# Kernel tuning notes

Hardware: AMD Instinct MI355X
Metric: run time of the kernel (lower is better)

The kernel has to match this reference:

```python
import jax, jax.numpy as jnp
import numpy as np

VOCAB, E, H = 100000, 300, 2048

def setup_inputs() -> dict:
    key = jax.random.key(0)
    k1, k2, k3, k4, k5, k6 = jax.random.split(key, 6)
    s_e = 1.0 / np.sqrt(H)
    return {
        "input": jax.random.randint(k1, (128, 64), 0, VOCAB),
        "embed": jax.random.normal(k2, (VOCAB, E), dtype=jnp.float32),
        "w_ih": jax.random.normal(k3, (4 * H, E), dtype=jnp.float32) * s_e,
        "w_hh": jax.random.normal(k4, (4 * H, H), dtype=jnp.float32) * s_e,
        "b_ih": jax.random.normal(k5, (4 * H,), dtype=jnp.float32) * s_e,
        "b_hh": jax.random.normal(k6, (4 * H,), dtype=jnp.float32) * s_e,
    }

def _lstm_cell(x, h, c, w_ih, w_hh, b_ih, b_hh):
    # PyTorch LSTMCell: gates = x @ W_ih^T + b_ih + h @ W_hh^T + b_hh
    gates = x @ w_ih.T + b_ih + h @ w_hh.T + b_hh  # [B, 4H]
    i, f, g, o = jnp.split(gates, 4, axis=-1)
    i, f, o = jax.nn.sigmoid(i), jax.nn.sigmoid(f), jax.nn.sigmoid(o)
    g = jnp.tanh(g)
    c_new = f * c + i * g
    h_new = o * jnp.tanh(c_new)
    return h_new, c_new

def reference(input, embed, w_ih, w_hh, b_ih, b_hh):
    B, T = input.shape
    x = embed[input]  # [B, T, E] embedding lookup
    x_t = jnp.swapaxes(x, 0, 1)  # [T, B, E] for scan over time
    h0 = jnp.zeros((B, H), dtype=x.dtype)
    c0 = jnp.zeros((B, H), dtype=x.dtype)

    def step(carry, xt):
        h, c = carry
        h, c = _lstm_cell(xt, h, c, w_ih, w_hh, b_ih, b_hh)
        return (h, c), None

    (hT, cT), _ = jax.lax.scan(step, (h0, c0), x_t)
    return hT  # [B, H]
```

## Files before the change

### kernel.cpp

```cpp
#include <hip/hip_runtime.h>
#include <stdint.h>

#define H_    2048
#define B_    128
#define T_    64
#define E_    300
#define NKU   76
#define XGRP  48
#define NWG   256
#define NTHR  512

typedef unsigned short u16;
typedef uint32_t u32;
typedef short bf8 __attribute__((ext_vector_type(8)));
typedef float f4 __attribute__((ext_vector_type(4)));

__device__ __forceinline__ u16 f2b(float f) {
    u32 u = __float_as_uint(f);
    u += 0x7fffu + ((u >> 16) & 1u);
    return (u16)(u >> 16);
}
__device__ __forceinline__ float sigm(float x) { return 1.f / (1.f + __expf(-x)); }
__device__ __forceinline__ float tanh_(float x) {
    float xx = fminf(fmaxf(x, -15.f), 15.f);
    float e = __expf(2.f * xx);
    return (e - 1.f) / (e + 1.f);
}

__global__ void prep_kernel(const float* __restrict__ w_hh, const float* __restrict__ w_ih,
                            const float* __restrict__ b_ih, const float* __restrict__ b_hh,
                            u16* __restrict__ wP, float* __restrict__ bsP,
                            float* __restrict__ cP, u16* __restrict__ hP0) {
    int tid = blockIdx.x * blockDim.x + threadIdx.x;
    int np = gridDim.x * blockDim.x;
    const int NF = NWG * NKU * 2 * 64;
    for (int f = tid; f < NF; f += np) {
        int lane = f & 63;
        int fr = f >> 6;
        int nt = fr & 1;
        int rest = fr >> 1;
        int ku = rest % NKU;
        int wg = rest / NKU;
        int l15 = lane & 15, q = lane >> 4;
        int nl = nt * 16 + l15;
        int g = nl & 3, jj = nl >> 2;
        int ng = g * H_ + wg * 8 + jj;
        int k0 = ku * 32 + q * 8;
        union { u16 s[8]; uint4 v; } tmp;
#pragma unroll
        for (int j = 0; j < 8; ++j) {
            int k = k0 + j;
            float v;
            if (k < H_) v = w_hh[(size_t)ng * H_ + k];
            else { int kx = k - H_; v = (kx < E_) ? w_ih[(size_t)ng * E_ + kx] : 0.f; }
            tmp.s[j] = f2b(v);
        }
        *(uint4*)&wP[(size_t)f * 8] = tmp.v;
    }
    for (int n = tid; n < 4 * H_; n += np) {
        int wg = n >> 5, nl = n & 31;
        int jj = nl >> 2, g = nl & 3;
        int src = g * H_ + wg * 8 + jj;
        bsP[n] = b_ih[src] + b_hh[src];
    }
    for (int i = tid; i < NWG * B_ * 8; i += np) cP[i] = 0.f;
    for (int i = tid; i < (H_ / 8) * B_ * 8 / 2; i += np) ((u32*)hP0)[i] = 0u;
}

__global__ void gather_kernel(const int* __restrict__ input, const float* __restrict__ embed,
                              u16* __restrict__ xP) {
    int t = blockIdx.x;
    u16* xt = xP + (size_t)t * XGRP * B_ * 8;
    for (int id = threadIdx.x; id < XGRP * B_; id += blockDim.x) {
        int b = id & (B_ - 1);
        int gx = id >> 7;
        int row = input[b * T_ + t];
        const float* src = embed + (size_t)row * E_;
        union { u16 s[8]; uint4 v; } tmp;
#pragma unroll
        for (int j = 0; j < 8; ++j) {
            int k = gx * 8 + j;
            tmp.s[j] = (k < E_) ? f2b(src[k]) : (u16)0;
        }
        *(uint4*)&xt[(size_t)id * 8] = tmp.v;
    }
}

__global__ __launch_bounds__(NTHR) void
step_kernel(const u16* __restrict__ wP, const float* __restrict__ bsP,
            const u16* __restrict__ xt, const u16* __restrict__ hin,
            u16* __restrict__ hout, float* __restrict__ cP,
            float* __restrict__ outp) {
    __shared__ float bufs[8][32][36];
    int tid = threadIdx.x;
    int wid = tid >> 6, lane = tid & 63;
    int l15 = lane & 15, q = lane >> 4;
    int wg = blockIdx.x;

    int cnt = (wid < 4) ? 10 : 9;
    int ks  = (wid < 4) ? wid * 10 : 40 + (wid - 4) * 9;

    const u16* wbase = wP + (size_t)wg * NKU * 1024 + lane * 8;
    int hoff = q * 1024 + l15 * 8;

    f4 acc[2][8];
#pragma unroll
    for (int nt = 0; nt < 2; ++nt)
#pragma unroll
        for (int mt = 0; mt < 8; ++mt) acc[nt][mt] = (f4)0.f;

#define LDF(KU, WF, HB) do {                                                  \
        int ku_ = (KU);                                                       \
        const u16* wb_ = wbase + (size_t)ku_ * 1024;                          \
        WF[0] = *(const bf8*)wb_;                                             \
        WF[1] = *(const bf8*)(wb_ + 512);                                     \
        const u16* hb_ = ((ku_ < 64) ? (hin + (size_t)ku_ * 4096)             \
                                     : (xt + (size_t)(ku_ - 64) * 4096)) + hoff; \
        _Pragma("unroll")                                                     \
        for (int mt_ = 0; mt_ < 8; ++mt_) HB[mt_] = *(const bf8*)(hb_ + mt_ * 128); \
    } while (0)

#define MM(WF, HB) do {                                                       \
        _Pragma("unroll")                                                     \
        for (int mt_ = 0; mt_ < 8; ++mt_) {                                   \
            acc[0][mt_] = __builtin_amdgcn_mfma_f32_16x16x32_bf16(WF[0], HB[mt_], acc[0][mt_], 0, 0, 0); \
            acc[1][mt_] = __builtin_amdgcn_mfma_f32_16x16x32_bf16(WF[1], HB[mt_], acc[1][mt_], 0, 0, 0); \
        }                                                                     \
    } while (0)

    bf8 wfA[2], hbA[8], wfB[2], hbB[8];
    LDF(ks, wfA, hbA);
    int i = 0;
    while (true) {
        if (i + 1 < cnt) LDF(ks + i + 1, wfB, hbB);
        MM(wfA, hbA);
        if (i + 1 >= cnt) break;
        if (i + 2 < cnt) LDF(ks + i + 2, wfA, hbA);
        MM(wfB, hbB);
        if (i + 2 >= cnt) break;
        i += 2;
    }
#undef LDF
#undef MM

    int cjj = tid & 7, cml = (tid >> 3) & 31;
    f4 bsv = {0.f, 0.f, 0.f, 0.f};
    if (tid < 256) bsv = *(const f4*)&bsP[wg * 32 + cjj * 4];
#pragma unroll
    for (int p = 0; p < 4; ++p) {
        __syncthreads();
#pragma unroll
        for (int mh = 0; mh < 2; ++mh) {
            int mt = p * 2 + mh;
            int ml = mh * 16 + l15;
            *(f4*)&bufs[wid][ml][q * 4]      = acc[0][mt];
            *(f4*)&bufs[wid][ml][16 + q * 4] = acc[1][mt];
        }
        __syncthreads();
        if (tid < 256) {
            int m = p * 32 + cml;
            f4 s = {0.f, 0.f, 0.f, 0.f};
#pragma unroll
            for (int kp = 0; kp < 8; ++kp) {
                f4 v = *(const f4*)&bufs[kp][cml][cjj * 4];
                s[0] += v[0]; s[1] += v[1]; s[2] += v[2]; s[3] += v[3];
            }
            float iv = sigm(s[0] + bsv[0]);
            float fv = sigm(s[1] + bsv[1]);
            float gv = tanh_(s[2] + bsv[2]);
            float ov = sigm(s[3] + bsv[3]);
            size_t ci = ((size_t)wg * B_ + m) * 8 + cjj;
            float cn = fv * cP[ci] + iv * gv;
            cP[ci] = cn;
            float hn = ov * tanh_(cn);
            hout[ci] = f2b(hn);
            if (outp) outp[(size_t)m * H_ + wg * 8 + cjj] = hn;
        }
    }
}

extern "C" void kernel_launch(void* const* d_in, const int* in_sizes, int n_in,
                              void* d_out, int out_size, void* d_ws, size_t ws_size,
                              hipStream_t stream) {
    const int*   input = (const int*)d_in[0];
    const float* embed = (const float*)d_in[1];
    const float* w_ih  = (const float*)d_in[2];
    const float* w_hh  = (const float*)d_in[3];
    const float* b_ih  = (const float*)d_in[4];
    const float* b_hh  = (const float*)d_in[5];
    float* out = (float*)d_out;

    char* ws = (char*)d_ws;
    size_t o = 0;
    u16* wP   = (u16*)(ws + o); o += (size_t)NWG * NKU * 2 * 64 * 8 * 2;
    u16* xP   = (u16*)(ws + o); o += (size_t)T_ * XGRP * B_ * 8 * 2;
    u16* hP0  = (u16*)(ws + o); o += (size_t)(H_ / 8) * B_ * 8 * 2;
    u16* hP1  = (u16*)(ws + o); o += (size_t)(H_ / 8) * B_ * 8 * 2;
    float* cP = (float*)(ws + o); o += (size_t)NWG * B_ * 8 * 4;
    float* bsP = (float*)(ws + o); o += (size_t)4 * H_ * 4;

    prep_kernel<<<2048, 256, 0, stream>>>(w_hh, w_ih, b_ih, b_hh, wP, bsP, cP, hP0);
    gather_kernel<<<T_, 256, 0, stream>>>(input, embed, xP);

    for (int t = 0; t < T_; ++t) {
        const u16* hin = (t & 1) ? hP1 : hP0;
        u16* hout      = (t & 1) ? hP0 : hP1;
        float* hof     = (t == T_ - 1) ? out : nullptr;
        step_kernel<<<NWG, NTHR, 0, stream>>>(
            wP, bsP, xP + (size_t)t * XGRP * B_ * 8, hin, hout, cP, hof);
    }
}
```

Baseline: 1.127 ms.

## Retile LSTM step to 64 gate columns by 64 batch rows per workgroup

```diff
diff --git a/kernel.cpp b/kernel.cpp
--- a/kernel.cpp
+++ b/kernel.cpp
@@ -9,6 +9,7 @@
 #define XGRP  48
 #define NWG   256
 #define NTHR  512
+#define NJG   128
 
 typedef unsigned short u16;
 typedef uint32_t u32;
@@ -33,18 +34,18 @@
                             float* __restrict__ cP, u16* __restrict__ hP0) {
     int tid = blockIdx.x * blockDim.x + threadIdx.x;
     int np = gridDim.x * blockDim.x;
-    const int NF = NWG * NKU * 2 * 64;
+    const int NF = NJG * NKU * 4 * 64;
     for (int f = tid; f < NF; f += np) {
         int lane = f & 63;
         int fr = f >> 6;
-        int nt = fr & 1;
-        int rest = fr >> 1;
+        int nt = fr & 3;
+        int rest = fr >> 2;
         int ku = rest % NKU;
-        int wg = rest / NKU;
+        int jg = rest / NKU;
         int l15 = lane & 15, q = lane >> 4;
         int nl = nt * 16 + l15;
         int g = nl & 3, jj = nl >> 2;
-        int ng = g * H_ + wg * 8 + jj;
+        int ng = g * H_ + jg * 16 + jj;
         int k0 = ku * 32 + q * 8;
         union { u16 s[8]; uint4 v; } tmp;
 #pragma unroll
@@ -57,13 +58,13 @@
         }
         *(uint4*)&wP[(size_t)f * 8] = tmp.v;
     }
-    for (int n = tid; n < 4 * H_; n += np) {
-        int wg = n >> 5, nl = n & 31;
-        int jj = nl >> 2, g = nl & 3;
-        int src = g * H_ + wg * 8 + jj;
+    for (int n = tid; n < NJG * 64; n += np) {
+        int jg = n >> 6, r = n & 63;
+        int jj = r >> 2, g = r & 3;
+        int src = g * H_ + jg * 16 + jj;
         bsP[n] = b_ih[src] + b_hh[src];
     }
-    for (int i = tid; i < NWG * B_ * 8; i += np) cP[i] = 0.f;
+    for (int i = tid; i < NJG * B_ * 16; i += np) cP[i] = 0.f;
     for (int i = tid; i < (H_ / 8) * B_ * 8 / 2; i += np) ((u32*)hP0)[i] = 0u;
 }
 
@@ -91,90 +92,98 @@
             const u16* __restrict__ xt, const u16* __restrict__ hin,
             u16* __restrict__ hout, float* __restrict__ cP,
             float* __restrict__ outp) {
-    __shared__ float bufs[8][32][36];
+    __shared__ float bufs[8][16][68];
     int tid = threadIdx.x;
     int wid = tid >> 6, lane = tid & 63;
     int l15 = lane & 15, q = lane >> 4;
-    int wg = blockIdx.x;
+    int jg  = blockIdx.x & 127;
+    int wgm = blockIdx.x >> 7;
 
     int cnt = (wid < 4) ? 10 : 9;
     int ks  = (wid < 4) ? wid * 10 : 40 + (wid - 4) * 9;
 
-    const u16* wbase = wP + (size_t)wg * NKU * 1024 + lane * 8;
-    int hoff = q * 1024 + l15 * 8;
-
-    f4 acc[2][8];
-#pragma unroll
-    for (int nt = 0; nt < 2; ++nt)
-#pragma unroll
-        for (int mt = 0; mt < 8; ++mt) acc[nt][mt] = (f4)0.f;
+    const u16* wbase = wP + (size_t)jg * NKU * 2048 + lane * 8;
+    int hoff = q * 1024 + wgm * 512 + l15 * 8;
+
+    f4 acc[4][4];
+#pragma unroll
+    for (int nt = 0; nt < 4; ++nt)
+#pragma unroll
+        for (int mt = 0; mt < 4; ++mt) acc[nt][mt] = (f4)0.f;
 
 #define LDF(KU, WF, HB) do {                                                  \
         int ku_ = (KU);                                                       \
-        const u16* wb_ = wbase + (size_t)ku_ * 1024;                          \
-        WF[0] = *(const bf8*)wb_;                                             \
+        const u16* wb_ = wbase + (size_t)ku_ * 2048;                          \
+        WF[0] = *(const bf8*)(wb_);                                           \
         WF[1] = *(const bf8*)(wb_ + 512);                                     \
+        WF[2] = *(const bf8*)(wb_ + 1024);                                    \
+        WF[3] = *(const bf8*)(wb_ + 1536);                                    \
         const u16* hb_ = ((ku_ < 64) ? (hin + (size_t)ku_ * 4096)             \
                                      : (xt + (size_t)(ku_ - 64) * 4096)) + hoff; \
-        _Pragma("unroll")                                                     \
-        for (int mt_ = 0; mt_ < 8; ++mt_) HB[mt_] = *(const bf8*)(hb_ + mt_ * 128); \
+        HB[0] = *(const bf8*)(hb_);                                           \
+        HB[1] = *(const bf8*)(hb_ + 128);                                     \
+        HB[2] = *(const bf8*)(hb_ + 256);                                     \
+        HB[3] = *(const bf8*)(hb_ + 384);                                     \
     } while (0)
 
 #define MM(WF, HB) do {                                                       \
         _Pragma("unroll")                                                     \
-        for (int mt_ = 0; mt_ < 8; ++mt_) {                                   \
-            acc[0][mt_] = __builtin_amdgcn_mfma_f32_16x16x32_bf16(WF[0], HB[mt_], acc[0][mt_], 0, 0, 0); \
-            acc[1][mt_] = __builtin_amdgcn_mfma_f32_16x16x32_bf16(WF[1], HB[mt_], acc[1][mt_], 0, 0, 0); \
-        }                                                                     \
+        for (int nt_ = 0; nt_ < 4; ++nt_)                                     \
+            _Pragma("unroll")                                                 \
+            for (int mt_ = 0; mt_ < 4; ++mt_)                                 \
+                acc[nt_][mt_] = __builtin_amdgcn_mfma_f32_16x16x32_bf16(      \
+                    WF[nt_], HB[mt_], acc[nt_][mt_], 0, 0, 0);                \
     } while (0)
 
-    bf8 wfA[2], hbA[8], wfB[2], hbB[8];
-    LDF(ks, wfA, hbA);
+    bf8 wA[4], hA[4], wB[4], hB[4], wC[4], hC[4];
+    LDF(ks, wA, hA);
+    LDF(ks + 1, wB, hB);
     int i = 0;
     while (true) {
-        if (i + 1 < cnt) LDF(ks + i + 1, wfB, hbB);
-        MM(wfA, hbA);
+        if (i + 2 < cnt) LDF(ks + i + 2, wC, hC);
+        MM(wA, hA);
         if (i + 1 >= cnt) break;
-        if (i + 2 < cnt) LDF(ks + i + 2, wfA, hbA);
-        MM(wfB, hbB);
+        if (i + 3 < cnt) LDF(ks + i + 3, wA, hA);
+        MM(wB, hB);
         if (i + 2 >= cnt) break;
-        i += 2;
+        if (i + 4 < cnt) LDF(ks + i + 4, wB, hB);
+        MM(wC, hC);
+        if (i + 3 >= cnt) break;
+        i += 3;
     }
 #undef LDF
 #undef MM
 
-    int cjj = tid & 7, cml = (tid >> 3) & 31;
+    int jj = tid & 15, ml16 = (tid >> 4) & 15;
     f4 bsv = {0.f, 0.f, 0.f, 0.f};
-    if (tid < 256) bsv = *(const f4*)&bsP[wg * 32 + cjj * 4];
+    if (tid < 256) bsv = *(const f4*)&bsP[jg * 64 + jj * 4];
 #pragma unroll
     for (int p = 0; p < 4; ++p) {
         __syncthreads();
-#pragma unroll
-        for (int mh = 0; mh < 2; ++mh) {
-            int mt = p * 2 + mh;
-            int ml = mh * 16 + l15;
-            *(f4*)&bufs[wid][ml][q * 4]      = acc[0][mt];
-            *(f4*)&bufs[wid][ml][16 + q * 4] = acc[1][mt];
-        }
+        *(f4*)&bufs[wid][l15][0 * 16 + q * 4] = acc[0][p];
+        *(f4*)&bufs[wid][l15][1 * 16 + q * 4] = acc[1][p];
+        *(f4*)&bufs[wid][l15][2 * 16 + q * 4] = acc[2][p];
+        *(f4*)&bufs[wid][l15][3 * 16 + q * 4] = acc[3][p];
         __syncthreads();
         if (tid < 256) {
-            int m = p * 32 + cml;
             f4 s = {0.f, 0.f, 0.f, 0.f};
 #pragma unroll
-            for (int kp = 0; kp < 8; ++kp) {
-                f4 v = *(const f4*)&bufs[kp][cml][cjj * 4];
+            for (int w = 0; w < 8; ++w) {
+                f4 v = *(const f4*)&bufs[w][ml16][jj * 4];
                 s[0] += v[0]; s[1] += v[1]; s[2] += v[2]; s[3] += v[3];
             }
             float iv = sigm(s[0] + bsv[0]);
             float fv = sigm(s[1] + bsv[1]);
             float gv = tanh_(s[2] + bsv[2]);
             float ov = sigm(s[3] + bsv[3]);
-            size_t ci = ((size_t)wg * B_ + m) * 8 + cjj;
+            int m = wgm * 64 + p * 16 + ml16;
+            size_t ci = ((size_t)jg * B_ + m) * 16 + jj;
             float cn = fv * cP[ci] + iv * gv;
             cP[ci] = cn;
             float hn = ov * tanh_(cn);
-            hout[ci] = f2b(hn);
-            if (outp) outp[(size_t)m * H_ + wg * 8 + cjj] = hn;
+            int jglob = jg * 16 + jj;
+            hout[(size_t)(jglob >> 3) * 1024 + m * 8 + (jglob & 7)] = f2b(hn);
+            if (outp) outp[(size_t)m * H_ + jglob] = hn;
         }
     }
 }
@@ -192,11 +201,11 @@
 
     char* ws = (char*)d_ws;
     size_t o = 0;
-    u16* wP   = (u16*)(ws + o); o += (size_t)NWG * NKU * 2 * 64 * 8 * 2;
+    u16* wP   = (u16*)(ws + o); o += (size_t)NJG * NKU * 4 * 64 * 8 * 2;
     u16* xP   = (u16*)(ws + o); o += (size_t)T_ * XGRP * B_ * 8 * 2;
     u16* hP0  = (u16*)(ws + o); o += (size_t)(H_ / 8) * B_ * 8 * 2;
     u16* hP1  = (u16*)(ws + o); o += (size_t)(H_ / 8) * B_ * 8 * 2;
-    float* cP = (float*)(ws + o); o += (size_t)NWG * B_ * 8 * 4;
+    float* cP = (float*)(ws + o); o += (size_t)NJG * B_ * 16 * 4;
     float* bsP = (float*)(ws + o); o += (size_t)4 * H_ * 4;
 
     prep_kernel<<<2048, 256, 0, stream>>>(w_hh, w_ih, b_ih, b_hh, wP, bsP, cP, hP0);
```

Result: faster. 1.074 ms (-4.7%).

## Fuse all timesteps into one persistent cooperative kernel with register-resident weights

Applied to the files above, without the earlier changes.

```diff
diff --git a/kernel.cpp b/kernel.cpp
--- a/kernel.cpp
+++ b/kernel.cpp
@@ -30,7 +30,7 @@
 __global__ void prep_kernel(const float* __restrict__ w_hh, const float* __restrict__ w_ih,
                             const float* __restrict__ b_ih, const float* __restrict__ b_hh,
                             u16* __restrict__ wP, float* __restrict__ bsP,
-                            float* __restrict__ cP, u16* __restrict__ hP0) {
+                            u16* __restrict__ hP0, unsigned* __restrict__ bar) {
     int tid = blockIdx.x * blockDim.x + threadIdx.x;
     int np = gridDim.x * blockDim.x;
     const int NF = NWG * NKU * 2 * 64;
@@ -57,14 +57,14 @@
         }
         *(uint4*)&wP[(size_t)f * 8] = tmp.v;
     }
-    for (int n = tid; n < 4 * H_; n += np) {
+    for (int n = tid; n < NWG * 32; n += np) {
         int wg = n >> 5, nl = n & 31;
         int jj = nl >> 2, g = nl & 3;
         int src = g * H_ + wg * 8 + jj;
         bsP[n] = b_ih[src] + b_hh[src];
     }
-    for (int i = tid; i < NWG * B_ * 8; i += np) cP[i] = 0.f;
     for (int i = tid; i < (H_ / 8) * B_ * 8 / 2; i += np) ((u32*)hP0)[i] = 0u;
+    for (int i = tid; i < 144; i += np) bar[i] = 0u;
 }
 
 __global__ void gather_kernel(const int* __restrict__ input, const float* __restrict__ embed,
@@ -86,12 +86,13 @@
     }
 }
 
-__global__ __launch_bounds__(NTHR) void
-step_kernel(const u16* __restrict__ wP, const float* __restrict__ bsP,
-            const u16* __restrict__ xt, const u16* __restrict__ hin,
-            u16* __restrict__ hout, float* __restrict__ cP,
-            float* __restrict__ outp) {
+__global__ __launch_bounds__(NTHR, 2) void
+lstm_persist(const u16* __restrict__ xb, const u16* __restrict__ wP,
+             const float* __restrict__ bsP, u16* __restrict__ h0,
+             u16* __restrict__ h1, unsigned* __restrict__ bar,
+             float* __restrict__ outp) {
     __shared__ float bufs[8][32][36];
+    __shared__ float cst[B_][8];
     int tid = threadIdx.x;
     int wid = tid >> 6, lane = tid & 63;
     int l15 = lane & 15, q = lane >> 4;
@@ -100,81 +101,123 @@
     int cnt = (wid < 4) ? 10 : 9;
     int ks  = (wid < 4) ? wid * 10 : 40 + (wid - 4) * 9;
 
-    const u16* wbase = wP + (size_t)wg * NKU * 1024 + lane * 8;
+    bf8 Wf[10][2];
+#pragma unroll
+    for (int i = 0; i < 10; ++i)
+        if (i < cnt) {
+            const u16* wb = wP + ((size_t)(wg * NKU + ks + i) * 2) * 512 + lane * 8;
+            Wf[i][0] = *(const bf8*)wb;
+            Wf[i][1] = *(const bf8*)(wb + 512);
+        }
+
     int hoff = q * 1024 + l15 * 8;
 
-    f4 acc[2][8];
-#pragma unroll
-    for (int nt = 0; nt < 2; ++nt)
-#pragma unroll
-        for (int mt = 0; mt < 8; ++mt) acc[nt][mt] = (f4)0.f;
-
-#define LDF(KU, WF, HB) do {                                                  \
+    int cjj0 = (tid & 3) * 2, cml = (tid >> 2) & 31;
+    f4 bv0 = {0,0,0,0}, bv1 = {0,0,0,0};
+    if (tid < 128) {
+        bv0 = *(const f4*)&bsP[wg * 32 + cjj0 * 4];
+        bv1 = *(const f4*)&bsP[wg * 32 + cjj0 * 4 + 4];
+    }
+    for (int i = tid; i < B_ * 8; i += NTHR) ((float*)cst)[i] = 0.f;
+
+    for (int t = 0; t < T_; ++t) {
+        const u16* hin = (t & 1) ? h1 : h0;
+        u16* hout      = (t & 1) ? h0 : h1;
+        const u16* xt = xb + (size_t)t * (XGRP * B_ * 8);
+
+        f4 acc[2][8];
+#pragma unroll
+        for (int nt = 0; nt < 2; ++nt)
+#pragma unroll
+            for (int mt = 0; mt < 8; ++mt) acc[nt][mt] = (f4)0.f;
+
+#define LDH(KU, HB_) do {                                                     \
         int ku_ = (KU);                                                       \
-        const u16* wb_ = wbase + (size_t)ku_ * 1024;                          \
-        WF[0] = *(const bf8*)wb_;                                             \
-        WF[1] = *(const bf8*)(wb_ + 512);                                     \
         const u16* hb_ = ((ku_ < 64) ? (hin + (size_t)ku_ * 4096)             \
                                      : (xt + (size_t)(ku_ - 64) * 4096)) + hoff; \
         _Pragma("unroll")                                                     \
-        for (int mt_ = 0; mt_ < 8; ++mt_) HB[mt_] = *(const bf8*)(hb_ + mt_ * 128); \
+        for (int mt_ = 0; mt_ < 8; ++mt_) HB_[mt_] = *(const bf8*)(hb_ + mt_ * 128); \
     } while (0)
 
-#define MM(WF, HB) do {                                                       \
+#define MM2(WI, HB_) do {                                                     \
         _Pragma("unroll")                                                     \
         for (int mt_ = 0; mt_ < 8; ++mt_) {                                   \
-            acc[0][mt_] = __builtin_amdgcn_mfma_f32_16x16x32_bf16(WF[0], HB[mt_], acc[0][mt_], 0, 0, 0); \
-            acc[1][mt_] = __builtin_amdgcn_mfma_f32_16x16x32_bf16(WF[1], HB[mt_], acc[1][mt_], 0, 0, 0); \
+            acc[0][mt_] = __builtin_amdgcn_mfma_f32_16x16x32_bf16(Wf[WI][0], HB_[mt_], acc[0][mt_], 0, 0, 0); \
+            acc[1][mt_] = __builtin_amdgcn_mfma_f32_16x16x32_bf16(Wf[WI][1], HB_[mt_], acc[1][mt_], 0, 0, 0); \
         }                                                                     \
     } while (0)
 
-    bf8 wfA[2], hbA[8], wfB[2], hbB[8];
-    LDF(ks, wfA, hbA);
-    int i = 0;
-    while (true) {
-        if (i + 1 < cnt) LDF(ks + i + 1, wfB, hbB);
-        MM(wfA, hbA);
-        if (i + 1 >= cnt) break;
-        if (i + 2 < cnt) LDF(ks + i + 2, wfA, hbA);
-        MM(wfB, hbB);
-        if (i + 2 >= cnt) break;
-        i += 2;
-    }
-#undef LDF
-#undef MM
-
-    int cjj = tid & 7, cml = (tid >> 3) & 31;
-    f4 bsv = {0.f, 0.f, 0.f, 0.f};
-    if (tid < 256) bsv = *(const f4*)&bsP[wg * 32 + cjj * 4];
-#pragma unroll
-    for (int p = 0; p < 4; ++p) {
-        __syncthreads();
-#pragma unroll
-        for (int mh = 0; mh < 2; ++mh) {
-            int mt = p * 2 + mh;
-            int ml = mh * 16 + l15;
-            *(f4*)&bufs[wid][ml][q * 4]      = acc[0][mt];
-            *(f4*)&bufs[wid][ml][16 + q * 4] = acc[1][mt];
-        }
-        __syncthreads();
-        if (tid < 256) {
-            int m = p * 32 + cml;
-            f4 s = {0.f, 0.f, 0.f, 0.f};
-#pragma unroll
-            for (int kp = 0; kp < 8; ++kp) {
-                f4 v = *(const f4*)&bufs[kp][cml][cjj * 4];
-                s[0] += v[0]; s[1] += v[1]; s[2] += v[2]; s[3] += v[3];
+        bf8 hA[8], hB[8];
+        LDH(ks, hA);
+#pragma unroll
+        for (int i = 0; i < 10; i += 2) {
+            if (i >= cnt) break;
+            if (i + 1 < cnt) LDH(ks + i + 1, hB);
+            MM2(i, hA);
+            if (i + 1 >= cnt) break;
+            if (i + 2 < cnt) LDH(ks + i + 2, hA);
+            MM2(i + 1, hB);
+        }
+#undef LDH
+#undef MM2
+
+        bool last = (t == T_ - 1);
+#pragma unroll
+        for (int p = 0; p < 4; ++p) {
+            __syncthreads();
+#pragma unroll
+            for (int mh = 0; mh < 2; ++mh) {
+                int mt = p * 2 + mh;
+                *(f4*)&bufs[wid][mh * 16 + l15][q * 4]      = acc[0][mt];
+                *(f4*)&bufs[wid][mh * 16 + l15][16 + q * 4] = acc[1][mt];
             }
-            float iv = sigm(s[0] + bsv[0]);
-            float fv = sigm(s[1] + bsv[1]);
-            float gv = tanh_(s[2] + bsv[2]);
-            float ov = sigm(s[3] + bsv[3]);
-            size_t ci = ((size_t)wg * B_ + m) * 8 + cjj;
-            float cn = fv * cP[ci] + iv * gv;
-            cP[ci] = cn;
-            float hn = ov * tanh_(cn);
-            hout[ci] = f2b(hn);
-            if (outp) outp[(size_t)m * H_ + wg * 8 + cjj] = hn;
+            __syncthreads();
+            if (tid < 128) {
+                int m = p * 32 + cml;
+                f4 s0 = {0,0,0,0}, s1 = {0,0,0,0};
+#pragma unroll
+                for (int w = 0; w < 8; ++w) {
+                    f4 v0 = *(const f4*)&bufs[w][cml][cjj0 * 4];
+                    f4 v1 = *(const f4*)&bufs[w][cml][cjj0 * 4 + 4];
+                    s0[0] += v0[0]; s0[1] += v0[1]; s0[2] += v0[2]; s0[3] += v0[3];
+                    s1[0] += v1[0]; s1[1] += v1[1]; s1[2] += v1[2]; s1[3] += v1[3];
+                }
+                float i0 = sigm(s0[0] + bv0[0]), f0 = sigm(s0[1] + bv0[1]);
+                float g0 = tanh_(s0[2] + bv0[2]), o0 = sigm(s0[3] + bv0[3]);
+                float i1 = sigm(s1[0] + bv1[0]), f1 = sigm(s1[1] + bv1[1]);
+                float g1 = tanh_(s1[2] + bv1[2]), o1 = sigm(s1[3] + bv1[3]);
+                float c0 = f0 * cst[m][cjj0] + i0 * g0;
+                float c1 = f1 * cst[m][cjj0 + 1] + i1 * g1;
+                cst[m][cjj0] = c0;
+                cst[m][cjj0 + 1] = c1;
+                float hn0 = o0 * tanh_(c0);
+                float hn1 = o1 * tanh_(c1);
+                ((u32*)hout)[wg * 512 + m * 4 + (cjj0 >> 1)] =
+                    (u32)f2b(hn0) | ((u32)f2b(hn1) << 16);
+                if (last) {
+                    float2 ov = {hn0, hn1};
+                    *(float2*)&outp[(size_t)m * H_ + wg * 8 + cjj0] = ov;
+                }
+            }
+        }
+
+        if (t < T_ - 1) {
+            __syncthreads();
+            if (tid == 0) {
+                __threadfence();
+                unsigned old = __hip_atomic_fetch_add(&bar[(wg & 7) * 16], 1u,
+                                   __ATOMIC_RELAXED, __HIP_MEMORY_SCOPE_AGENT);
+                if (old == 32u * (unsigned)(t + 1) - 1u)
+                    __hip_atomic_fetch_add(&bar[128], 1u,
+                        __ATOMIC_RELAXED, __HIP_MEMORY_SCOPE_AGENT);
+                unsigned tgt = 8u * (unsigned)(t + 1);
+                while (__hip_atomic_load(&bar[128], __ATOMIC_RELAXED,
+                                         __HIP_MEMORY_SCOPE_AGENT) < tgt)
+                    __builtin_amdgcn_s_sleep(1);
+                (void)__hip_atomic_load(&bar[128], __ATOMIC_ACQUIRE,
+                                        __HIP_MEMORY_SCOPE_AGENT);
+            }
+            __syncthreads();
         }
     }
 }
@@ -192,21 +235,19 @@
 
     char* ws = (char*)d_ws;
     size_t o = 0;
-    u16* wP   = (u16*)(ws + o); o += (size_t)NWG * NKU * 2 * 64 * 8 * 2;
+    u16* wP   = (u16*)(ws + o); o += (size_t)NWG * NKU * 2 * 512 * 2;
     u16* xP   = (u16*)(ws + o); o += (size_t)T_ * XGRP * B_ * 8 * 2;
     u16* hP0  = (u16*)(ws + o); o += (size_t)(H_ / 8) * B_ * 8 * 2;
     u16* hP1  = (u16*)(ws + o); o += (size_t)(H_ / 8) * B_ * 8 * 2;
-    float* cP = (float*)(ws + o); o += (size_t)NWG * B_ * 8 * 4;
-    float* bsP = (float*)(ws + o); o += (size_t)4 * H_ * 4;
-
-    prep_kernel<<<2048, 256, 0, stream>>>(w_hh, w_ih, b_ih, b_hh, wP, bsP, cP, hP0);
+    float* bsP = (float*)(ws + o); o += (size_t)NWG * 32 * 4;
+    o = (o + 255) & ~(size_t)255;
+    unsigned* bar = (unsigned*)(ws + o); o += 144 * 4;
+
+    prep_kernel<<<2048, 256, 0, stream>>>(w_hh, w_ih, b_ih, b_hh, wP, bsP, hP0, bar);
     gather_kernel<<<T_, 256, 0, stream>>>(input, embed, xP);
 
-    for (int t = 0; t < T_; ++t) {
-        const u16* hin = (t & 1) ? hP1 : hP0;
-        u16* hout      = (t & 1) ? hP0 : hP1;
-        float* hof     = (t == T_ - 1) ? out : nullptr;
-        step_kernel<<<NWG, NTHR, 0, stream>>>(
-            wP, bsP, xP + (size_t)t * XGRP * B_ * 8, hin, hout, cP, hof);
-    }
-}
+    void* kargs[] = {(void*)&xP, (void*)&wP, (void*)&bsP,
+                     (void*)&hP0, (void*)&hP1, (void*)&bar, (void*)&out};
+    hipLaunchCooperativeKernel((void*)lstm_persist, dim3(NWG), dim3(NTHR),
+                               kargs, 0, stream);
+}
```

New measurement: 1.714 ms. 1.52x slower.
